# Optimization experiments

Hardware: AMD Instinct MI355X
Metric: run time of the kernel (lower is better)

Reference implementation:

```python
import math
import jax, jax.numpy as jnp
import numpy as np

B, L, D, H = 2, 2048, 1024, 16
DT = D // H  # 64


def setup_inputs() -> dict:
    key = jax.random.key(0)
    ks = jax.random.split(key, 11)
    s = 1.0 / math.sqrt(D)
    return {
        "q": jax.random.normal(ks[0], (B, L, D), jnp.float32),
        "k": jax.random.normal(ks[1], (B, L, D), jnp.float32),
        "v": jax.random.normal(ks[2], (B, L, D), jnp.float32),
        "Wq": jax.random.normal(ks[3], (D, D), jnp.float32) * s,
        "bq": jnp.zeros((D,), jnp.float32),
        "Wk": jax.random.normal(ks[4], (D, D), jnp.float32) * s,
        "bk": jnp.zeros((D,), jnp.float32),
        "Wv": jax.random.normal(ks[5], (D, D), jnp.float32) * s,
        "bv": jnp.zeros((D,), jnp.float32),
        "Wc": jax.random.normal(ks[6], (D, D), jnp.float32) * s,
        "bc": jnp.zeros((D,), jnp.float32),
    }


def reference(q, k, v, Wq, bq, Wk, bk, Wv, bv, Wc, bc):
    # Linear projections (torch Linear: x @ W^T + b)
    Q = q @ Wq.T + bq
    K = k @ Wk.T + bk
    V = v @ Wv.T + bv
    # split(): plain view/reshape [B, L, D] -> [B, H, L, d] (faithful to source)
    Qs = Q.reshape(B, H, L, DT)
    Ks = K.reshape(B, H, L, DT)
    Vs = V.reshape(B, H, L, DT)
    # k_t is also a plain reshape [B,H,L,d] -> [B,H,d,L] (NOT a transpose)
    Kt = Ks.reshape(B, H, DT, L)
    score = jnp.matmul(Qs, Kt) / math.sqrt(DT)  # [B, H, L, L]
    # nn.Softmax() with no dim on 4D tensor -> legacy dim=1 (head axis)
    attn = jax.nn.softmax(score, axis=1)
    out = jnp.matmul(attn, Vs)  # [B, H, L, d]
    out = out.reshape(B, L, D)  # concat() is also a plain reshape
    return out @ Wc.T + bc
```

## Files before the change

kernel.cpp:

```cpp
#include <hip/hip_runtime.h>
#include <hip/hip_bf16.h>


using u16   = unsigned short;
using f16   = _Float16;
using f16x2 = _Float16 __attribute__((ext_vector_type(2)));
using f16x8 = _Float16 __attribute__((ext_vector_type(8)));
using bf16x8 = __bf16 __attribute__((ext_vector_type(8)));
using f32x4  = float  __attribute__((ext_vector_type(4)));

__device__ __forceinline__ u16 f2bf(float f) {
    __bf16 h = (__bf16)f;
    return __builtin_bit_cast(u16, h);
}
__device__ __forceinline__ float ex2(float x) {
    return __builtin_amdgcn_exp2f(x);
}
__device__ __forceinline__ bf16x8 ldfrag(const u16* p) {
    bf16x8 r; __builtin_memcpy(&r, p, 16); return r;
}
__device__ __forceinline__ f16x8 ldfrag16(const u16* p) {
    f16x8 r; __builtin_memcpy(&r, p, 16); return r;
}
__device__ __forceinline__ unsigned pkrtz(float a, float b) {
    return __builtin_bit_cast(unsigned, __builtin_amdgcn_cvt_pkrtz(a, b));
}
__device__ __forceinline__ f16x2 u2h(unsigned u) { return __builtin_bit_cast(f16x2, u); }
__device__ __forceinline__ unsigned h2u(f16x2 h) { return __builtin_bit_cast(unsigned, h); }

__device__ __forceinline__ void stage16(const float* p, u16* d) {
    #pragma unroll
    for (int u = 0; u < 16; u += 4) {
        float4 t = *reinterpret_cast<const float4*>(p + u);
        d[u + 0] = f2bf(t.x); d[u + 1] = f2bf(t.y);
        d[u + 2] = f2bf(t.z); d[u + 3] = f2bf(t.w);
    }
}
__device__ __forceinline__ void stage16(const u16* p, u16* d) {
    #pragma unroll
    for (int u = 0; u < 16; u += 8)
        *reinterpret_cast<uint4*>(d + u) = *reinterpret_cast<const uint4*>(p + u);
}
template <int NS>
__device__ __forceinline__ void stage16s(const u16* a, const u16* b,
                                         const u16* c, const u16* d2, u16* dst) {
    #pragma unroll
    for (int u = 0; u < 16; u += 8) {
        bf16x8 va = ldfrag(a + u), vb, vc, vd;
        if constexpr (NS >= 2) vb = ldfrag(b + u);
        if constexpr (NS >= 3) vc = ldfrag(c + u);
        if constexpr (NS >= 4) vd = ldfrag(d2 + u);
        #pragma unroll
        for (int e = 0; e < 8; ++e) {
            float s = (float)va[e];
            if constexpr (NS >= 2) s += (float)vb[e];
            if constexpr (NS >= 3) s += (float)vc[e];
            if constexpr (NS >= 4) s += (float)vd[e];
            dst[u + e] = f2bf(s);
        }
    }
}

template <typename XT, typename OT, int NS, bool F16O>
__device__ __forceinline__ void gemm_body(
    const XT* __restrict__ X, const XT* __restrict__ X2,
    const XT* __restrict__ X3, const XT* __restrict__ X4,
    const float* __restrict__ W, const float* __restrict__ bias,
    OT* __restrict__ C, float scale,
    u16 (*lX)[72], u16 (*lW)[72])
{
    const int tid  = threadIdx.x;
    const int lane = tid & 63;
    const int wv   = tid >> 6;
    const int wm   = (wv >> 2) * 64;
    const int wn   = (wv & 3) * 32;
    const int m0 = blockIdx.x * 128;
    const int n0 = blockIdx.y * 128;
    const int sr = tid >> 2;
    const int sq = (tid & 3) * 16;
    const int fm = lane & 15;
    const int g  = lane >> 4;
    const int fk = g * 8;

    f32x4 acc[4][2] = {};

    for (int k0 = 0; k0 < 1024; k0 += 64) {
        {
            const size_t xo = (size_t)(m0 + sr) * 1024 + k0 + sq;
            if constexpr (NS > 1)
                stage16s<NS>(X + xo, X2 + xo, X3 + xo, X4 + xo, &lX[sr][sq]);
            else
                stage16(X + xo, &lX[sr][sq]);
        }
        stage16(W + (size_t)(n0 + sr) * 1024 + k0 + sq, &lW[sr][sq]);
        __syncthreads();
        #pragma unroll
        for (int kb = 0; kb < 2; ++kb) {
            bf16x8 a[4], bb[2];
            #pragma unroll
            for (int mb = 0; mb < 4; ++mb)
                a[mb] = ldfrag(&lX[wm + mb * 16 + fm][kb * 32 + fk]);
            #pragma unroll
            for (int nb = 0; nb < 2; ++nb)
                bb[nb] = ldfrag(&lW[wn + nb * 16 + fm][kb * 32 + fk]);
            #pragma unroll
            for (int mb = 0; mb < 4; ++mb)
                #pragma unroll
                for (int nb = 0; nb < 2; ++nb)
                    acc[mb][nb] = __builtin_amdgcn_mfma_f32_16x16x32_bf16(
                        a[mb], bb[nb], acc[mb][nb], 0, 0, 0);
        }
        __syncthreads();
    }

    #pragma unroll
    for (int mb = 0; mb < 4; ++mb) {
        #pragma unroll
        for (int nb = 0; nb < 2; ++nb) {
            const int row = m0 + wm + mb * 16 + g * 4;
            const int col = n0 + wn + nb * 16 + fm;
            const float bv = bias[col];
            #pragma unroll
            for (int r = 0; r < 4; ++r) {
                const float val = (acc[mb][nb][r] + bv) * scale;
                OT* p = C + (size_t)(row + r) * 1024 + col;
                if constexpr (F16O) {
                    f16 h = (f16)val;
                    *p = __builtin_bit_cast(u16, h);
                } else if constexpr (__is_same(OT, u16)) {
                    *p = f2bf(val);
                } else {
                    *p = val;
                }
            }
        }
    }
}

__global__ __launch_bounds__(512) void gemm_qkv(
    const float* __restrict__ q, const float* __restrict__ k,
    const float* __restrict__ v,
    const float* __restrict__ Wq, const float* __restrict__ bq,
    const float* __restrict__ Wk, const float* __restrict__ bk,
    const float* __restrict__ Wv, const float* __restrict__ bv,
    u16* __restrict__ Q16, u16* __restrict__ K16, u16* __restrict__ V16,
    float qscale)
{
    __shared__ u16 lX[128][72];
    __shared__ u16 lW[128][72];
    const int z = blockIdx.z;
    const float* X = (z == 0) ? q  : (z == 1) ? k  : v;
    const float* W = (z == 0) ? Wq : (z == 1) ? Wk : Wv;
    const float* B = (z == 0) ? bq : (z == 1) ? bk : bv;
    u16*         C = (z == 0) ? Q16 : (z == 1) ? K16 : V16;
    const float  s = (z == 0) ? qscale : 1.0f;
    gemm_body<float, u16, 1, true>(X, nullptr, nullptr, nullptr, W, B, C, s, lX, lW);
}

template <int NS>
__global__ __launch_bounds__(512) void gemm_final(
    const u16* __restrict__ X, const u16* __restrict__ X2,
    const u16* __restrict__ X3, const u16* __restrict__ X4,
    const float* __restrict__ W, const float* __restrict__ bias,
    float* __restrict__ C)
{
    __shared__ u16 lX[128][72];
    __shared__ u16 lW[128][72];
    gemm_body<u16, float, NS, false>(X, X2, X3, X4, W, bias, C, 1.0f, lX, lW);
}

__global__ __launch_bounds__(256) void tp_kv2(
    const u16* __restrict__ kin, u16* __restrict__ kout,
    const u16* __restrict__ vin, u16* __restrict__ vout)
{
    __shared__ u16 t[64][80];
    const int which = (blockIdx.x >> 10) & 1;
    const int bx    = blockIdx.x & 1023;
    const u16* in_  = which ? vin  : kin;
    u16*       out_ = which ? vout : kout;
    const int tid = threadIdx.x;
    const int bh  = bx >> 5;
    const int tt  = bx & 31;
    const size_t base = (size_t)bh * 131072;
    const int C         = which ? 64 : 2048;
    const int r0        = which ? tt * 64 : 0;
    const int c0        = which ? 0 : tt * 64;
    const int outstride = which ? 2048 : 64;
    const u16* in = in_ + base;
    u16* out      = out_ + base;

    #pragma unroll
    for (int half = 0; half < 2; ++half) {
        const int rr = (tid >> 3) + half * 32;
        const int cb = tid & 7;
        const int cbs = cb ^ ((rr >> 3) & 7);
        *reinterpret_cast<uint4*>(&t[rr][cbs * 8]) =
            *reinterpret_cast<const uint4*>(in + (size_t)(r0 + rr) * C + c0 + cb * 8);
    }
    __syncthreads();
    #pragma unroll
    for (int half = 0; half < 2; ++half) {
        const int c  = (tid >> 3) + half * 32;
        const int rb = tid & 7;
        u16 vv[8];
        #pragma unroll
        for (int e = 0; e < 8; ++e) {
            const int r = rb * 8 + e;
            const int cbs2 = (c >> 3) ^ ((r >> 3) & 7);
            vv[e] = t[r][cbs2 * 8 + (c & 7)];
        }
        *reinterpret_cast<uint4*>(out + (size_t)(c0 + c) * outstride + r0 + rb * 8) =
            *reinterpret_cast<uint4*>(vv);
    }
}

__global__ __launch_bounds__(1024) void attn_fused(
    const u16* __restrict__ Qb, const u16* __restrict__ KT,
    const u16* __restrict__ VT, u16* __restrict__ O0,
    u16* __restrict__ O1, u16* __restrict__ O2, u16* __restrict__ O3,
    int jsplit)
{
    __shared__ unsigned expS[16][64][20];
    __shared__ unsigned rcpS[64][20];

    const int tid  = threadIdx.x;
    const int w    = tid >> 6;
    const int lane = tid & 63;
    const int fm   = lane & 15;
    const int g    = lane >> 4;
    const int fk   = g * 8;
    const int g4   = g * 4;
    const int g2   = g * 2;

    int b, it, js;
    u16* Ob;
    if (jsplit == 4) {
        const int grp = blockIdx.x & 7;
        b  = grp >> 2;
        js = grp & 3;
        it = blockIdx.x >> 3;
        Ob = (js == 0) ? O0 : (js == 1) ? O1 : (js == 2) ? O2 : O3;
    } else if (jsplit == 2) {
        const int grp = blockIdx.x & 3;
        b  = grp >> 1;
        js = grp & 1;
        it = blockIdx.x >> 2;
        Ob = js ? O1 : O0;
    } else {
        b  = blockIdx.x >> 5;
        it = blockIdx.x & 31;
        js = 0;
        Ob = O0;
    }
    const int jlen  = 2048 / jsplit;
    const int jbase = js * jlen;
    const int i0    = it * 64;
    const size_t hb = ((size_t)b * 2048 + (size_t)w * 128) * 1024;

    f16x8 qa[4][2];
    #pragma unroll
    for (int m = 0; m < 4; ++m)
        #pragma unroll
        for (int kb = 0; kb < 2; ++kb)
            qa[m][kb] = ldfrag16(Qb + hb + (size_t)(i0 + m * 16 + fm) * 64 + kb * 32 + fk);

    f32x4 oacc[4][4] = {};

    const int nt  = jlen >> 5;

    auto qk_tile = [&](int j0) {
        f16x8 kf[2][2];
        #pragma unroll
        for (int kb = 0; kb < 2; ++kb)
            #pragma unroll
            for (int nb = 0; nb < 2; ++nb)
                kf[kb][nb] = ldfrag16(KT + hb + (size_t)(j0 + nb * 16 + fm) * 64
                                               + kb * 32 + fk);
        #pragma unroll
        for (int m = 0; m < 4; ++m) {
            f32x4 st[2] = {};
            #pragma unroll
            for (int kb = 0; kb < 2; ++kb)
                #pragma unroll
                for (int nb = 0; nb < 2; ++nb)
                    st[nb] = __builtin_amdgcn_mfma_f32_16x16x32_f16(
                        kf[kb][nb], qa[m][kb], st[nb], 0, 0, 0);
            const int row = m * 16 + fm;
            #pragma unroll
            for (int nb = 0; nb < 2; ++nb) {
                uint2 ew2;
                ew2.x = pkrtz(ex2(st[nb][0]), ex2(st[nb][1]));
                ew2.y = pkrtz(ex2(st[nb][2]), ex2(st[nb][3]));
                *reinterpret_cast<uint2*>(&expS[w][row][nb * 8 + g2]) = ew2;
            }
        }
    };

    qk_tile(jbase);

    for (int t = 0; t < nt; ++t) {
        const int j0 = jbase + (t << 5);
        __syncthreads();
        f16x8 vf[4];
        #pragma unroll
        for (int nb = 0; nb < 4; ++nb)
            vf[nb] = ldfrag16(VT + hb + (size_t)(nb * 16 + fm) * 2048 + j0 + fk);
        {
            const int i  = tid >> 4;
            const int jp = tid & 15;
            unsigned eh[16];
            #pragma unroll
            for (int h = 0; h < 16; ++h) eh[h] = expS[h][i][jp];
            const f16x2 s0 = (u2h(eh[0])  + u2h(eh[1]))  + (u2h(eh[2])  + u2h(eh[3]));
            const f16x2 s1 = (u2h(eh[4])  + u2h(eh[5]))  + (u2h(eh[6])  + u2h(eh[7]));
            const f16x2 s2 = (u2h(eh[8])  + u2h(eh[9]))  + (u2h(eh[10]) + u2h(eh[11]));
            const f16x2 s3 = (u2h(eh[12]) + u2h(eh[13])) + (u2h(eh[14]) + u2h(eh[15]));
            const f16x2 ts = (s0 + s1) + (s2 + s3);
            rcpS[i][jp] = pkrtz(__builtin_amdgcn_rcpf((float)ts[0]),
                                __builtin_amdgcn_rcpf((float)ts[1]));
        }
        __syncthreads();
        #pragma unroll
        for (int m = 0; m < 4; ++m) {
            const int row = m * 16 + fm;
            const uint4 ew = *reinterpret_cast<const uint4*>(&expS[w][row][g4]);
            const uint4 rw = *reinterpret_cast<const uint4*>(&rcpS[row][g4]);
            uint4 pw;
            pw.x = h2u(u2h(ew.x) * u2h(rw.x));
            pw.y = h2u(u2h(ew.y) * u2h(rw.y));
            pw.z = h2u(u2h(ew.z) * u2h(rw.z));
            pw.w = h2u(u2h(ew.w) * u2h(rw.w));
            const f16x8 pa = __builtin_bit_cast(f16x8, pw);
            #pragma unroll
            for (int nb = 0; nb < 4; ++nb)
                oacc[m][nb] = __builtin_amdgcn_mfma_f32_16x16x32_f16(
                    pa, vf[nb], oacc[m][nb], 0, 0, 0);
        }
        if (t + 1 < nt) qk_tile(j0 + 32);
    }

    #pragma unroll
    for (int m = 0; m < 4; ++m)
        #pragma unroll
        for (int nb = 0; nb < 4; ++nb)
            #pragma unroll
            for (int r = 0; r < 4; ++r) {
                const int i = i0 + m * 16 + g4 + r;
                Ob[hb + (size_t)i * 64 + nb * 16 + fm] = f2bf(oacc[m][nb][r]);
            }
}

extern "C" void kernel_launch(void* const* d_in, const int* in_sizes, int n_in,
                              void* d_out, int out_size, void* d_ws, size_t ws_size,
                              hipStream_t stream)
{
    const float* q  = (const float*)d_in[0];
    const float* k  = (const float*)d_in[1];
    const float* v  = (const float*)d_in[2];
    const float* Wq = (const float*)d_in[3];
    const float* bq = (const float*)d_in[4];
    const float* Wk = (const float*)d_in[5];
    const float* bk = (const float*)d_in[6];
    const float* Wv = (const float*)d_in[7];
    const float* bv = (const float*)d_in[8];
    const float* Wc = (const float*)d_in[9];
    const float* bc = (const float*)d_in[10];
    float* out = (float*)d_out;

    const size_t MD = (size_t)4096 * 1024;
    u16* W0 = (u16*)d_ws;
    u16* W1 = W0 + MD;
    u16* W2 = W1 + MD;
    u16* W3 = W2 + MD;
    u16* W4 = W3 + MD;
    u16* W5 = W4 + MD;
    u16* W6 = W5 + MD;

    int jsplit = 1;
    if      (ws_size >= 7 * MD * sizeof(u16)) jsplit = 4;
    else if (ws_size >= 5 * MD * sizeof(u16)) jsplit = 2;

    const float qscale = 0.125f * 1.4426950408889634f;

    gemm_qkv<<<dim3(32, 8, 3), dim3(512), 0, stream>>>(
        q, k, v, Wq, bq, Wk, bk, Wv, bv, W0, W1, W2, qscale);
    tp_kv2<<<dim3(2048), dim3(256), 0, stream>>>(W1, W3, W2, W4);
    const int agrid = (jsplit == 4) ? 256 : (jsplit == 2) ? 128 : 64;
    attn_fused<<<dim3(agrid), dim3(1024), 0, stream>>>(
        W0, W3, W4, W1, W2, W5, W6, jsplit);
    if (jsplit == 4)
        gemm_final<4><<<dim3(32, 8), dim3(512), 0, stream>>>(W1, W2, W5, W6, Wc, bc, out);
    else if (jsplit == 2)
        gemm_final<2><<<dim3(32, 8), dim3(512), 0, stream>>>(W1, W2, nullptr, nullptr, Wc, bc, out);
    else
        gemm_final<1><<<dim3(32, 8), dim3(512), 0, stream>>>(W1, nullptr, nullptr, nullptr, Wc, bc, out);
}
```

Baseline: 214.1 us.

## Double-buffer exp/reciprocal LDS tiles and XOR-swizzle to halve barriers

```diff
diff --git a/kernel.cpp b/kernel.cpp
--- a/kernel.cpp
+++ b/kernel.cpp
@@ -220,8 +220,8 @@
     u16* __restrict__ O1, u16* __restrict__ O2, u16* __restrict__ O3,
     int jsplit)
 {
-    __shared__ unsigned expS[16][64][20];
-    __shared__ unsigned rcpS[64][20];
+    __shared__ unsigned expS[2][16][64][16];
+    __shared__ unsigned rcpS[2][64][16];
 
     const int tid  = threadIdx.x;
     const int w    = tid >> 6;
@@ -257,6 +257,8 @@
     const int i0    = it * 64;
     const size_t hb = ((size_t)b * 2048 + (size_t)w * 128) * 1024;
 
+    auto fx = [](int r) { return ((r >> 1) & 3) << 2; };
+
     f16x8 qa[4][2];
     #pragma unroll
     for (int m = 0; m < 4; ++m)
@@ -268,7 +270,7 @@
 
     const int nt  = jlen >> 5;
 
-    auto qk_tile = [&](int j0) {
+    auto qk_tile = [&](int j0, int bf) {
         f16x8 kf[2][2];
         #pragma unroll
         for (int kb = 0; kb < 2; ++kb)
@@ -286,45 +288,43 @@
                     st[nb] = __builtin_amdgcn_mfma_f32_16x16x32_f16(
                         kf[kb][nb], qa[m][kb], st[nb], 0, 0, 0);
             const int row = m * 16 + fm;
+            const int fr  = fx(row);
             #pragma unroll
             for (int nb = 0; nb < 2; ++nb) {
                 uint2 ew2;
                 ew2.x = pkrtz(ex2(st[nb][0]), ex2(st[nb][1]));
                 ew2.y = pkrtz(ex2(st[nb][2]), ex2(st[nb][3]));
-                *reinterpret_cast<uint2*>(&expS[w][row][nb * 8 + g2]) = ew2;
+                *reinterpret_cast<uint2*>(&expS[bf][w][row][(nb * 8 + g2) ^ fr]) = ew2;
             }
         }
     };
 
-    qk_tile(jbase);
-
-    for (int t = 0; t < nt; ++t) {
-        const int j0 = jbase + (t << 5);
-        __syncthreads();
+    auto sum_tile = [&](int bf) {
+        const int i  = tid >> 4;
+        const int jp = (tid & 15) ^ fx(i);
+        unsigned eh[16];
+        #pragma unroll
+        for (int h = 0; h < 16; ++h) eh[h] = expS[bf][h][i][jp];
+        const f16x2 s0 = (u2h(eh[0])  + u2h(eh[1]))  + (u2h(eh[2])  + u2h(eh[3]));
+        const f16x2 s1 = (u2h(eh[4])  + u2h(eh[5]))  + (u2h(eh[6])  + u2h(eh[7]));
+        const f16x2 s2 = (u2h(eh[8])  + u2h(eh[9]))  + (u2h(eh[10]) + u2h(eh[11]));
+        const f16x2 s3 = (u2h(eh[12]) + u2h(eh[13])) + (u2h(eh[14]) + u2h(eh[15]));
+        const f16x2 ts = (s0 + s1) + (s2 + s3);
+        rcpS[bf][i][jp] = pkrtz(__builtin_amdgcn_rcpf((float)ts[0]),
+                                __builtin_amdgcn_rcpf((float)ts[1]));
+    };
+
+    auto pv_tile = [&](int j0, int bf) {
         f16x8 vf[4];
         #pragma unroll
         for (int nb = 0; nb < 4; ++nb)
             vf[nb] = ldfrag16(VT + hb + (size_t)(nb * 16 + fm) * 2048 + j0 + fk);
-        {
-            const int i  = tid >> 4;
-            const int jp = tid & 15;
-            unsigned eh[16];
-            #pragma unroll
-            for (int h = 0; h < 16; ++h) eh[h] = expS[h][i][jp];
-            const f16x2 s0 = (u2h(eh[0])  + u2h(eh[1]))  + (u2h(eh[2])  + u2h(eh[3]));
-            const f16x2 s1 = (u2h(eh[4])  + u2h(eh[5]))  + (u2h(eh[6])  + u2h(eh[7]));
-            const f16x2 s2 = (u2h(eh[8])  + u2h(eh[9]))  + (u2h(eh[10]) + u2h(eh[11]));
-            const f16x2 s3 = (u2h(eh[12]) + u2h(eh[13])) + (u2h(eh[14]) + u2h(eh[15]));
-            const f16x2 ts = (s0 + s1) + (s2 + s3);
-            rcpS[i][jp] = pkrtz(__builtin_amdgcn_rcpf((float)ts[0]),
-                                __builtin_amdgcn_rcpf((float)ts[1]));
-        }
-        __syncthreads();
         #pragma unroll
         for (int m = 0; m < 4; ++m) {
             const int row = m * 16 + fm;
-            const uint4 ew = *reinterpret_cast<const uint4*>(&expS[w][row][g4]);
-            const uint4 rw = *reinterpret_cast<const uint4*>(&rcpS[row][g4]);
+            const int fr  = fx(row);
+            const uint4 ew = *reinterpret_cast<const uint4*>(&expS[bf][w][row][g4 ^ fr]);
+            const uint4 rw = *reinterpret_cast<const uint4*>(&rcpS[bf][row][g4 ^ fr]);
             uint4 pw;
             pw.x = h2u(u2h(ew.x) * u2h(rw.x));
             pw.y = h2u(u2h(ew.y) * u2h(rw.y));
@@ -336,7 +336,19 @@
                 oacc[m][nb] = __builtin_amdgcn_mfma_f32_16x16x32_f16(
                     pa, vf[nb], oacc[m][nb], 0, 0, 0);
         }
-        if (t + 1 < nt) qk_tile(j0 + 32);
+    };
+
+    qk_tile(jbase, 0);
+    __syncthreads();
+    sum_tile(0);
+
+    for (int t = 0; t < nt; ++t) {
+        const int cur = t & 1, nxt = cur ^ 1;
+        const int j0 = jbase + (t << 5);
+        if (t + 1 < nt) qk_tile(j0 + 32, nxt);
+        __syncthreads();
+        if (t + 1 < nt) sum_tile(nxt);
+        pv_tile(j0, cur);
     }
 
     #pragma unroll
```

Measured after the change: 234.9 us. 1.1x slower.

## Double attention j-tile to 64 columns and XOR-swizzle shared exp/rcp buffers

Applied to the files above, without the earlier changes.

```diff
diff --git a/kernel.cpp b/kernel.cpp
--- a/kernel.cpp
+++ b/kernel.cpp
@@ -220,8 +220,8 @@
     u16* __restrict__ O1, u16* __restrict__ O2, u16* __restrict__ O3,
     int jsplit)
 {
-    __shared__ unsigned expS[16][64][20];
-    __shared__ unsigned rcpS[64][20];
+    __shared__ unsigned expS[16][64][32];
+    __shared__ unsigned rcpS[64][32];
 
     const int tid  = threadIdx.x;
     const int w    = tid >> 6;
@@ -257,6 +257,8 @@
     const int i0    = it * 64;
     const size_t hb = ((size_t)b * 2048 + (size_t)w * 128) * 1024;
 
+    auto fx = [](int r) { return ((r >> 1) & 3) << 2; };
+
     f16x8 qa[4][2];
     #pragma unroll
     for (int m = 0; m < 4; ++m)
@@ -266,9 +268,9 @@
 
     f32x4 oacc[4][4] = {};
 
-    const int nt  = jlen >> 5;
-
-    auto qk_tile = [&](int j0) {
+    const int nt = jlen >> 6;
+
+    auto qk_half = [&](int j0, int cb) {
         f16x8 kf[2][2];
         #pragma unroll
         for (int kb = 0; kb < 2; ++kb)
@@ -286,45 +288,28 @@
                     st[nb] = __builtin_amdgcn_mfma_f32_16x16x32_f16(
                         kf[kb][nb], qa[m][kb], st[nb], 0, 0, 0);
             const int row = m * 16 + fm;
+            const int fr  = fx(row);
             #pragma unroll
             for (int nb = 0; nb < 2; ++nb) {
                 uint2 ew2;
                 ew2.x = pkrtz(ex2(st[nb][0]), ex2(st[nb][1]));
                 ew2.y = pkrtz(ex2(st[nb][2]), ex2(st[nb][3]));
-                *reinterpret_cast<uint2*>(&expS[w][row][nb * 8 + g2]) = ew2;
+                *reinterpret_cast<uint2*>(&expS[w][row][(cb + nb * 8 + g2) ^ fr]) = ew2;
             }
         }
     };
 
-    qk_tile(jbase);
-
-    for (int t = 0; t < nt; ++t) {
-        const int j0 = jbase + (t << 5);
-        __syncthreads();
+    auto pv_half = [&](int jh, int cb) {
         f16x8 vf[4];
         #pragma unroll
         for (int nb = 0; nb < 4; ++nb)
-            vf[nb] = ldfrag16(VT + hb + (size_t)(nb * 16 + fm) * 2048 + j0 + fk);
-        {
-            const int i  = tid >> 4;
-            const int jp = tid & 15;
-            unsigned eh[16];
-            #pragma unroll
-            for (int h = 0; h < 16; ++h) eh[h] = expS[h][i][jp];
-            const f16x2 s0 = (u2h(eh[0])  + u2h(eh[1]))  + (u2h(eh[2])  + u2h(eh[3]));
-            const f16x2 s1 = (u2h(eh[4])  + u2h(eh[5]))  + (u2h(eh[6])  + u2h(eh[7]));
-            const f16x2 s2 = (u2h(eh[8])  + u2h(eh[9]))  + (u2h(eh[10]) + u2h(eh[11]));
-            const f16x2 s3 = (u2h(eh[12]) + u2h(eh[13])) + (u2h(eh[14]) + u2h(eh[15]));
-            const f16x2 ts = (s0 + s1) + (s2 + s3);
-            rcpS[i][jp] = pkrtz(__builtin_amdgcn_rcpf((float)ts[0]),
-                                __builtin_amdgcn_rcpf((float)ts[1]));
-        }
-        __syncthreads();
+            vf[nb] = ldfrag16(VT + hb + (size_t)(nb * 16 + fm) * 2048 + jh + fk);
         #pragma unroll
         for (int m = 0; m < 4; ++m) {
             const int row = m * 16 + fm;
-            const uint4 ew = *reinterpret_cast<const uint4*>(&expS[w][row][g4]);
-            const uint4 rw = *reinterpret_cast<const uint4*>(&rcpS[row][g4]);
+            const int fr  = fx(row);
+            const uint4 ew = *reinterpret_cast<const uint4*>(&expS[w][row][(cb + g4) ^ fr]);
+            const uint4 rw = *reinterpret_cast<const uint4*>(&rcpS[row][(cb + g4) ^ fr]);
             uint4 pw;
             pw.x = h2u(u2h(ew.x) * u2h(rw.x));
             pw.y = h2u(u2h(ew.y) * u2h(rw.y));
@@ -336,7 +321,45 @@
                 oacc[m][nb] = __builtin_amdgcn_mfma_f32_16x16x32_f16(
                     pa, vf[nb], oacc[m][nb], 0, 0, 0);
         }
-        if (t + 1 < nt) qk_tile(j0 + 32);
+    };
+
+    qk_half(jbase, 0);
+    qk_half(jbase + 32, 16);
+
+    for (int t = 0; t < nt; ++t) {
+        const int j0 = jbase + (t << 6);
+        __syncthreads();
+        {
+            const int i = tid >> 4;
+            const int p = (tid & 15) ^ fx(i);
+            unsigned e0[16], e1[16];
+            #pragma unroll
+            for (int h = 0; h < 16; ++h) {
+                e0[h] = expS[h][i][p];
+                e1[h] = expS[h][i][p + 16];
+            }
+            const f16x2 a0 = ((u2h(e0[0])  + u2h(e0[1]))  + (u2h(e0[2])  + u2h(e0[3])))
+                           + ((u2h(e0[4])  + u2h(e0[5]))  + (u2h(e0[6])  + u2h(e0[7])));
+            const f16x2 a1 = ((u2h(e0[8])  + u2h(e0[9]))  + (u2h(e0[10]) + u2h(e0[11])))
+                           + ((u2h(e0[12]) + u2h(e0[13])) + (u2h(e0[14]) + u2h(e0[15])));
+            const f16x2 ta = a0 + a1;
+            const f16x2 b0 = ((u2h(e1[0])  + u2h(e1[1]))  + (u2h(e1[2])  + u2h(e1[3])))
+                           + ((u2h(e1[4])  + u2h(e1[5]))  + (u2h(e1[6])  + u2h(e1[7])));
+            const f16x2 b1 = ((u2h(e1[8])  + u2h(e1[9]))  + (u2h(e1[10]) + u2h(e1[11])))
+                           + ((u2h(e1[12]) + u2h(e1[13])) + (u2h(e1[14]) + u2h(e1[15])));
+            const f16x2 tb = b0 + b1;
+            rcpS[i][p]      = pkrtz(__builtin_amdgcn_rcpf((float)ta[0]),
+                                    __builtin_amdgcn_rcpf((float)ta[1]));
+            rcpS[i][p + 16] = pkrtz(__builtin_amdgcn_rcpf((float)tb[0]),
+                                    __builtin_amdgcn_rcpf((float)tb[1]));
+        }
+        __syncthreads();
+        pv_half(j0, 0);
+        pv_half(j0 + 32, 16);
+        if (t + 1 < nt) {
+            qk_half(j0 + 64, 0);
+            qk_half(j0 + 96, 16);
+        }
     }
 
     #pragma unroll
```

Result: slower. 249.8 us (+16.7%).

## Pre-convert inputs and weights to bf16 and presum split attention partials

Applied to the files above, without the earlier changes.

```diff
diff --git a/kernel.cpp b/kernel.cpp
--- a/kernel.cpp
+++ b/kernel.cpp
@@ -41,31 +41,11 @@
     for (int u = 0; u < 16; u += 8)
         *reinterpret_cast<uint4*>(d + u) = *reinterpret_cast<const uint4*>(p + u);
 }
-template <int NS>
-__device__ __forceinline__ void stage16s(const u16* a, const u16* b,
-                                         const u16* c, const u16* d2, u16* dst) {
-    #pragma unroll
-    for (int u = 0; u < 16; u += 8) {
-        bf16x8 va = ldfrag(a + u), vb, vc, vd;
-        if constexpr (NS >= 2) vb = ldfrag(b + u);
-        if constexpr (NS >= 3) vc = ldfrag(c + u);
-        if constexpr (NS >= 4) vd = ldfrag(d2 + u);
-        #pragma unroll
-        for (int e = 0; e < 8; ++e) {
-            float s = (float)va[e];
-            if constexpr (NS >= 2) s += (float)vb[e];
-            if constexpr (NS >= 3) s += (float)vc[e];
-            if constexpr (NS >= 4) s += (float)vd[e];
-            dst[u + e] = f2bf(s);
-        }
-    }
-}
-
-template <typename XT, typename OT, int NS, bool F16O>
+
+template <typename XT, typename WT, typename OT, bool F16O>
 __device__ __forceinline__ void gemm_body(
-    const XT* __restrict__ X, const XT* __restrict__ X2,
-    const XT* __restrict__ X3, const XT* __restrict__ X4,
-    const float* __restrict__ W, const float* __restrict__ bias,
+    const XT* __restrict__ X,
+    const WT* __restrict__ W, const float* __restrict__ bias,
     OT* __restrict__ C, float scale,
     u16 (*lX)[72], u16 (*lW)[72])
 {
@@ -85,13 +65,7 @@
     f32x4 acc[4][2] = {};
 
     for (int k0 = 0; k0 < 1024; k0 += 64) {
-        {
-            const size_t xo = (size_t)(m0 + sr) * 1024 + k0 + sq;
-            if constexpr (NS > 1)
-                stage16s<NS>(X + xo, X2 + xo, X3 + xo, X4 + xo, &lX[sr][sq]);
-            else
-                stage16(X + xo, &lX[sr][sq]);
-        }
+        stage16(X + (size_t)(m0 + sr) * 1024 + k0 + sq, &lX[sr][sq]);
         stage16(W + (size_t)(n0 + sr) * 1024 + k0 + sq, &lW[sr][sq]);
         __syncthreads();
         #pragma unroll
@@ -137,36 +111,97 @@
     }
 }
 
-__global__ __launch_bounds__(512) void gemm_qkv(
-    const float* __restrict__ q, const float* __restrict__ k,
-    const float* __restrict__ v,
-    const float* __restrict__ Wq, const float* __restrict__ bq,
-    const float* __restrict__ Wk, const float* __restrict__ bk,
-    const float* __restrict__ Wv, const float* __restrict__ bv,
+template <typename T>
+__global__ __launch_bounds__(512) void gemm_qkv_t(
+    const T* __restrict__ q, const T* __restrict__ k,
+    const T* __restrict__ v,
+    const T* __restrict__ Wq, const float* __restrict__ bq,
+    const T* __restrict__ Wk, const float* __restrict__ bk,
+    const T* __restrict__ Wv, const float* __restrict__ bv,
     u16* __restrict__ Q16, u16* __restrict__ K16, u16* __restrict__ V16,
     float qscale)
 {
     __shared__ u16 lX[128][72];
     __shared__ u16 lW[128][72];
     const int z = blockIdx.z;
-    const float* X = (z == 0) ? q  : (z == 1) ? k  : v;
-    const float* W = (z == 0) ? Wq : (z == 1) ? Wk : Wv;
+    const T* X = (z == 0) ? q  : (z == 1) ? k  : v;
+    const T* W = (z == 0) ? Wq : (z == 1) ? Wk : Wv;
     const float* B = (z == 0) ? bq : (z == 1) ? bk : bv;
     u16*         C = (z == 0) ? Q16 : (z == 1) ? K16 : V16;
     const float  s = (z == 0) ? qscale : 1.0f;
-    gemm_body<float, u16, 1, true>(X, nullptr, nullptr, nullptr, W, B, C, s, lX, lW);
-}
-
-template <int NS>
-__global__ __launch_bounds__(512) void gemm_final(
-    const u16* __restrict__ X, const u16* __restrict__ X2,
-    const u16* __restrict__ X3, const u16* __restrict__ X4,
-    const float* __restrict__ W, const float* __restrict__ bias,
+    gemm_body<T, T, u16, true>(X, W, B, C, s, lX, lW);
+}
+
+template <typename WT>
+__global__ __launch_bounds__(512) void gemm_final_t(
+    const u16* __restrict__ X,
+    const WT* __restrict__ W, const float* __restrict__ bias,
     float* __restrict__ C)
 {
     __shared__ u16 lX[128][72];
     __shared__ u16 lW[128][72];
-    gemm_body<u16, float, NS, false>(X, X2, X3, X4, W, bias, C, 1.0f, lX, lW);
+    gemm_body<u16, WT, float, false>(X, W, bias, C, 1.0f, lX, lW);
+}
+
+__global__ __launch_bounds__(256) void prep_bf16(
+    const float* __restrict__ q, const float* __restrict__ k,
+    const float* __restrict__ v,
+    const float* __restrict__ Wq, const float* __restrict__ Wk,
+    const float* __restrict__ Wv, const float* __restrict__ Wc,
+    u16* __restrict__ qb, u16* __restrict__ kb, u16* __restrict__ vb,
+    u16* __restrict__ wqb, u16* __restrict__ wkb,
+    u16* __restrict__ wvb, u16* __restrict__ wcb)
+{
+    const long long NC = 2097152;
+    for (long long c = (long long)blockIdx.x * 256 + threadIdx.x; c < NC;
+         c += (long long)gridDim.x * 256) {
+        const float* src; u16* dst; long long off;
+        if (c < 1572864) {
+            if (c < 524288)       { src = q; dst = qb; off = c; }
+            else if (c < 1048576) { src = k; dst = kb; off = c - 524288; }
+            else                  { src = v; dst = vb; off = c - 1048576; }
+        } else {
+            const long long wI = c - 1572864;
+            if (wI < 131072)      { src = Wq; dst = wqb; off = wI; }
+            else if (wI < 262144) { src = Wk; dst = wkb; off = wI - 131072; }
+            else if (wI < 393216) { src = Wv; dst = wvb; off = wI - 262144; }
+            else                  { src = Wc; dst = wcb; off = wI - 393216; }
+        }
+        const float* p = src + off * 8;
+        const float4 a  = reinterpret_cast<const float4*>(p)[0];
+        const float4 b2 = reinterpret_cast<const float4*>(p)[1];
+        u16 d[8];
+        d[0] = f2bf(a.x);  d[1] = f2bf(a.y);  d[2] = f2bf(a.z);  d[3] = f2bf(a.w);
+        d[4] = f2bf(b2.x); d[5] = f2bf(b2.y); d[6] = f2bf(b2.z); d[7] = f2bf(b2.w);
+        *reinterpret_cast<uint4*>(dst + off * 8) = *reinterpret_cast<uint4*>(d);
+    }
+}
+
+template <int NS>
+__global__ __launch_bounds__(256) void presum_o(
+    const u16* __restrict__ a, const u16* __restrict__ b,
+    const u16* __restrict__ c, const u16* __restrict__ d,
+    u16* __restrict__ o)
+{
+    const long long NC = 524288;
+    for (long long i = (long long)blockIdx.x * 256 + threadIdx.x; i < NC;
+         i += (long long)gridDim.x * 256) {
+        const long long e0 = i * 8;
+        const bf16x8 va = ldfrag(a + e0);
+        const bf16x8 vb = ldfrag(b + e0);
+        bf16x8 vc, vd;
+        if constexpr (NS >= 3) vc = ldfrag(c + e0);
+        if constexpr (NS >= 4) vd = ldfrag(d + e0);
+        u16 r[8];
+        #pragma unroll
+        for (int e = 0; e < 8; ++e) {
+            float s = (float)va[e] + (float)vb[e];
+            if constexpr (NS >= 3) s += (float)vc[e];
+            if constexpr (NS >= 4) s += (float)vd[e];
+            r[e] = f2bf(s);
+        }
+        *reinterpret_cast<uint4*>(o + e0) = *reinterpret_cast<uint4*>(r);
+    }
 }
 
 __global__ __launch_bounds__(256) void tp_kv2(
@@ -368,6 +403,7 @@
     float* out = (float*)d_out;
 
     const size_t MD = (size_t)4096 * 1024;
+    const size_t WM = MD / 4;
     u16* W0 = (u16*)d_ws;
     u16* W1 = W0 + MD;
     u16* W2 = W1 + MD;
@@ -375,23 +411,49 @@
     u16* W4 = W3 + MD;
     u16* W5 = W4 + MD;
     u16* W6 = W5 + MD;
+    u16* qb  = W6 + MD;
+    u16* kb  = qb + MD;
+    u16* vb  = kb + MD;
+    u16* wqb = vb + MD;
+    u16* wkb = wqb + WM;
+    u16* wvb = wkb + WM;
+    u16* wcb = wvb + WM;
 
     int jsplit = 1;
     if      (ws_size >= 7 * MD * sizeof(u16)) jsplit = 4;
     else if (ws_size >= 5 * MD * sizeof(u16)) jsplit = 2;
+    const bool prep = ws_size >= 11 * MD * sizeof(u16);
 
     const float qscale = 0.125f * 1.4426950408889634f;
 
-    gemm_qkv<<<dim3(32, 8, 3), dim3(512), 0, stream>>>(
-        q, k, v, Wq, bq, Wk, bk, Wv, bv, W0, W1, W2, qscale);
+    if (prep)
+        prep_bf16<<<dim3(2048), dim3(256), 0, stream>>>(
+            q, k, v, Wq, Wk, Wv, Wc, qb, kb, vb, wqb, wkb, wvb, wcb);
+
+    if (prep)
+        gemm_qkv_t<u16><<<dim3(32, 8, 3), dim3(512), 0, stream>>>(
+            qb, kb, vb, wqb, bq, wkb, bk, wvb, bv, W0, W1, W2, qscale);
+    else
+        gemm_qkv_t<float><<<dim3(32, 8, 3), dim3(512), 0, stream>>>(
+            q, k, v, Wq, bq, Wk, bk, Wv, bv, W0, W1, W2, qscale);
+
     tp_kv2<<<dim3(2048), dim3(256), 0, stream>>>(W1, W3, W2, W4);
+
     const int agrid = (jsplit == 4) ? 256 : (jsplit == 2) ? 128 : 64;
     attn_fused<<<dim3(agrid), dim3(1024), 0, stream>>>(
         W0, W3, W4, W1, W2, W5, W6, jsplit);
-    if (jsplit == 4)
-        gemm_final<4><<<dim3(32, 8), dim3(512), 0, stream>>>(W1, W2, W5, W6, Wc, bc, out);
-    else if (jsplit == 2)
-        gemm_final<2><<<dim3(32, 8), dim3(512), 0, stream>>>(W1, W2, nullptr, nullptr, Wc, bc, out);
+
+    const u16* Xf = W1;
+    if (jsplit == 4) {
+        presum_o<4><<<dim3(2048), dim3(256), 0, stream>>>(W1, W2, W5, W6, W0);
+        Xf = W0;
+    } else if (jsplit == 2) {
+        presum_o<2><<<dim3(2048), dim3(256), 0, stream>>>(W1, W2, nullptr, nullptr, W0);
+        Xf = W0;
+    }
+
+    if (prep)
+        gemm_final_t<u16><<<dim3(32, 8), dim3(512), 0, stream>>>(Xf, wcb, bc, out);
     else
-        gemm_final<1><<<dim3(32, 8), dim3(512), 0, stream>>>(W1, nullptr, nullptr, nullptr, Wc, bc, out);
-}
+        gemm_final_t<float><<<dim3(32, 8), dim3(512), 0, stream>>>(Xf, Wc, bc, out);
+}
```

After: 184.2 us, median of 2. 1.16x faster.
